# Performance work log

Measured on AMD Instinct MI355X. Metric: run time of the kernel, lower is better.

## Reference

```python
import jax, jax.numpy as jnp
import numpy as np

B_SZ, L, H, N, OUT = 16, 4096, 128, 64, 128  # batch, seq, channels(input_dim), state(hidden_dim), output_dim


def _hippo_legs(n):
    # HiPPO-LegS matrix: A[i,k] = -sqrt(2i+1)sqrt(2k+1) for i>k, -(i+1) on diag, 0 above.
    q = np.sqrt(2 * np.arange(n) + 1.0)
    A = -np.tril(np.outer(q, q), -1) - np.diag(np.arange(n) + 1.0)
    return A.astype(np.float32)


def setup_inputs() -> dict:
    key = jax.random.key(0)
    k1, k2, k3, k4, k5, k6, k7 = jax.random.split(key, 7)
    x = jax.random.normal(k1, (B_SZ, L, H), dtype=jnp.float32)
    A = jnp.asarray(_hippo_legs(N))                                   # (N, N) fixed HiPPO
    Bm = jax.random.normal(k2, (H, N), dtype=jnp.float32)             # per-channel input matrix
    Cm = jax.random.normal(k3, (H, N), dtype=jnp.float32)             # per-channel output matrix
    D = jax.random.normal(k4, (H,), dtype=jnp.float32)                # skip/feedthrough
    # log-uniform timescales in [1e-3, 1e-1]
    log_dt = jnp.log(jnp.float32(1e-3)) + jax.random.uniform(k5, (H,), dtype=jnp.float32) * (
        jnp.log(jnp.float32(1e-1)) - jnp.log(jnp.float32(1e-3)))
    W = jax.random.normal(k6, (OUT, H), dtype=jnp.float32) / np.sqrt(H)  # Linear(in=H, out=OUT) weight
    b = jax.random.normal(k7, (OUT,), dtype=jnp.float32) * 0.01
    return {"x": x, "A": A, "Bm": Bm, "Cm": Cm, "D": D, "log_dt": log_dt, "W": W, "b": b}


def reference(x, A, Bm, Cm, D, log_dt, W, b):
    n = A.shape[0]
    seq_len = x.shape[1]
    dt = jnp.exp(log_dt)[:, None, None]            # (H,1,1)
    I = jnp.eye(n, dtype=x.dtype)
    lhs = I[None] - 0.5 * dt * A[None]             # (H,N,N)
    rhs = I[None] + 0.5 * dt * A[None]
    A_bar = jnp.linalg.solve(lhs, rhs)             # bilinear discretization, per channel
    B_bar = jnp.linalg.solve(lhs, (dt[:, :, 0] * Bm)[..., None])[..., 0]  # (H,N)

    # SSM convolution kernel k_l = C A_bar^l B_bar via scan, vectorized over channels.
    def step(V, _):
        k = jnp.einsum('hn,hn->h', Cm, V)
        V = jnp.einsum('hmn,hn->hm', A_bar, V)
        return V, k

    _, ks = jax.lax.scan(step, B_bar, None, length=seq_len)  # (L, H)
    kernel = ks.T                                            # (H, L)

    # Causal convolution via FFT (the 'fourier' method).
    n_fft = 2 * seq_len
    Uf = jnp.fft.rfft(x, n=n_fft, axis=1)                    # (B, F, H)
    Kf = jnp.fft.rfft(kernel, n=n_fft, axis=1)               # (H, F)
    y = jnp.fft.irfft(Uf * Kf.T[None], n=n_fft, axis=1)[:, :seq_len, :]
    y = y + x * D[None, None, :]

    return y @ W.T + b
```

## Files before the change

### kernel.cpp

```cpp
#include <hip/hip_runtime.h>

#define BSZ   16
#define LSEQ  4096
#define HCH   128
#define NST   64
#define NOUTD 128
#define TCH   64
#define NCHK  64

typedef unsigned long long u64;

#define OFF_XT 0ull
#define OFF_U  8388608ull
#define OFF_S  16777216ull
#define OFF_G  25165824ull
#define OFF_M  25690112ull
#define OFF_P  26214400ull
#define OFF_K  26738688ull
#define OFF_WT 26746880ull

__global__ __launch_bounds__(256) void k_tr_x(const float* __restrict__ x, float* __restrict__ xT){
  __shared__ float tile[64][65];
  int l0 = blockIdx.x*64, h0 = blockIdx.y*64, b = blockIdx.z;
  int tid = threadIdx.x;
  int tl = tid>>6, th = tid&63;
  #pragma unroll
  for (int k=0;k<16;k++){
    int l = tl + k*4;
    tile[l][th] = x[((u64)b*LSEQ + l0+l)*HCH + h0+th];
  }
  __syncthreads();
  #pragma unroll
  for (int k=0;k<16;k++){
    int hh = tl + k*4;
    xT[((u64)b*HCH + h0+hh)*LSEQ + l0+th] = tile[th][hh];
  }
}

__global__ __launch_bounds__(256) void k_tr_w(const float* __restrict__ W, float* __restrict__ Wt){
  int idx = blockIdx.x*256 + threadIdx.x;
  int o = idx >> 7, h = idx & 127;
  Wt[h*NOUTD + o] = W[o*HCH + h];
}

__global__ __launch_bounds__(512) void k_pre(const float* __restrict__ A, const float* __restrict__ Bm,
                   const float* __restrict__ Cm, const float* __restrict__ log_dt,
                   float* __restrict__ G, float* __restrict__ Mx,
                   float* __restrict__ P, float* __restrict__ ks){
  __shared__ __align__(16) float Ls [64][68];
  __shared__ __align__(16) float LsT[64][68];
  __shared__ __align__(16) float Bb [64][68];
  __shared__ __align__(16) float BbT[64][68];
  __shared__ __align__(16) float Vt [64][68];
  __shared__ __align__(16) float Wt [64][68];
  __shared__ float vbuf[64];
  __shared__ float cbuf[64];
  const int h = blockIdx.x, tid = threadIdx.x;
  const int lane = tid & 63, wid = tid >> 6;
  const float dt = expf(log_dt[h]);

  for (int i = tid; i < 4096; i += 512){
    int r = i >> 6, c = i & 63;
    Ls[r][c] = ((r==c)?1.f:0.f) - 0.5f*dt*A[i];
  }
  if (tid < 64) vbuf[tid] = Bm[h*NST + tid];
  else if (tid < 128) cbuf[tid-64] = Cm[h*NST + (tid-64)];
  __syncthreads();

  float y[64];
  if (wid == 0){
    const int t = lane;
    #pragma unroll
    for (int j=0;j<64;j++) y[j] = 0.f;
    #pragma unroll
    for (int i=0;i<64;i++){
      float acc = ((i==t)?2.f:0.f) - Ls[i][t];
      #pragma unroll
      for (int j4=0;j4<(i+3)/4;j4++){
        float4 L4 = *(const float4*)&Ls[i][j4*4];
        acc -= L4.x*y[j4*4+0] + L4.y*y[j4*4+1] + L4.z*y[j4*4+2] + L4.w*y[j4*4+3];
      }
      y[i] = acc * (1.0f/Ls[i][i]);
    }
    #pragma unroll
    for (int i=0;i<64;i++){ Ls[i][t] = y[i]; LsT[t][i] = y[i]; }
  }
  __syncthreads();

  if (wid == 0){
    const int t = lane;
    float a0=0.f,a1=0.f,a2=0.f,a3=0.f;
    #pragma unroll
    for (int m4=0;m4<16;m4++){
      float4 r4 = *(const float4*)&Ls[t][m4*4];
      a0 += r4.x*vbuf[m4*4+0]; a1 += r4.y*vbuf[m4*4+1];
      a2 += r4.z*vbuf[m4*4+2]; a3 += r4.w*vbuf[m4*4+3];
    }
    Vt[0][t] = 0.5f*dt*(((a0+a1)+(a2+a3)) + vbuf[t]);
  } else if (wid == 1){
    const int n = lane;
    float a0=0.f,a1=0.f,a2=0.f,a3=0.f;
    #pragma unroll
    for (int m4=0;m4<16;m4++){
      float4 c4 = *(const float4*)&LsT[n][m4*4];
      a0 += c4.x*cbuf[m4*4+0]; a1 += c4.y*cbuf[m4*4+1];
      a2 += c4.z*cbuf[m4*4+2]; a3 += c4.w*cbuf[m4*4+3];
    }
    Wt[0][n] = (a0+a1)+(a2+a3);
  }
  __syncthreads();

  float (*cur)[68]  = Ls,  (*curT)[68] = LsT;
  float (*nxt)[68]  = Bb,  (*nxtT)[68] = BbT;
  for (int k=0;k<6;k++){
    const int nv = 1<<k;
    for (int j = tid; j < 32*nv; j += 512){
      const int isW = (j >= 16*nv);
      const int jj  = isW ? (j - 16*nv) : j;
      const int i   = jj >> 4;
      const int n0  = (jj & 15) << 2;
      float (*Xs)[68] = isW ? Wt  : Vt;
      float (*Ms)[68] = isW ? cur : curT;
      float o0=0.f,o1=0.f,o2=0.f,o3=0.f;
      #pragma unroll
      for (int m4=0;m4<16;m4++){
        const float4 xv = *(const float4*)&Xs[i][m4*4];
        const float4 c0 = *(const float4*)&Ms[m4*4+0][n0];
        const float4 c1 = *(const float4*)&Ms[m4*4+1][n0];
        const float4 c2 = *(const float4*)&Ms[m4*4+2][n0];
        const float4 c3 = *(const float4*)&Ms[m4*4+3][n0];
        o0 += xv.x*c0.x + xv.y*c1.x + xv.z*c2.x + xv.w*c3.x;
        o1 += xv.x*c0.y + xv.y*c1.y + xv.z*c2.y + xv.w*c3.y;
        o2 += xv.x*c0.z + xv.y*c1.z + xv.z*c2.z + xv.w*c3.z;
        o3 += xv.x*c0.w + xv.y*c1.w + xv.z*c2.w + xv.w*c3.w;
      }
      float* dst = isW ? &Wt[nv+i][n0] : &Vt[nv+i][n0];
      *(float4*)dst = make_float4(o0,o1,o2,o3);
    }
    {
      const int ti = (tid >> 4) << 1;
      const int tj = (tid & 15) << 2;
      float acc[2][4] = {};
      #pragma unroll
      for (int m4=0;m4<16;m4++){
        const float4 a0 = *(const float4*)&cur[ti+0][m4*4];
        const float4 a1 = *(const float4*)&cur[ti+1][m4*4];
        const float4 b0 = *(const float4*)&cur[m4*4+0][tj];
        const float4 b1 = *(const float4*)&cur[m4*4+1][tj];
        const float4 b2 = *(const float4*)&cur[m4*4+2][tj];
        const float4 b3 = *(const float4*)&cur[m4*4+3][tj];
        acc[0][0] += a0.x*b0.x + a0.y*b1.x + a0.z*b2.x + a0.w*b3.x;
        acc[0][1] += a0.x*b0.y + a0.y*b1.y + a0.z*b2.y + a0.w*b3.y;
        acc[0][2] += a0.x*b0.z + a0.y*b1.z + a0.z*b2.z + a0.w*b3.z;
        acc[0][3] += a0.x*b0.w + a0.y*b1.w + a0.z*b2.w + a0.w*b3.w;
        acc[1][0] += a1.x*b0.x + a1.y*b1.x + a1.z*b2.x + a1.w*b3.x;
        acc[1][1] += a1.x*b0.y + a1.y*b1.y + a1.z*b2.y + a1.w*b3.y;
        acc[1][2] += a1.x*b0.z + a1.y*b1.z + a1.z*b2.z + a1.w*b3.z;
        acc[1][3] += a1.x*b0.w + a1.y*b1.w + a1.z*b2.w + a1.w*b3.w;
      }
      *(float4*)&nxt[ti+0][tj] = make_float4(acc[0][0],acc[0][1],acc[0][2],acc[0][3]);
      *(float4*)&nxt[ti+1][tj] = make_float4(acc[1][0],acc[1][1],acc[1][2],acc[1][3]);
      #pragma unroll
      for (int e=0;e<4;e++){
        nxtT[tj+e][ti+0] = acc[0][e];
        nxtT[tj+e][ti+1] = acc[1][e];
      }
    }
    __syncthreads();
    { float (*t0)[68]=cur; cur=nxt;  nxt=t0; }
    { float (*t1)[68]=curT; curT=nxtT; nxtT=t1; }
  }

  if (wid == 0){
    const int j = lane;
    float a0=0.f,a1=0.f,a2=0.f,a3=0.f;
    #pragma unroll
    for (int n4=0;n4<16;n4++){
      float4 v4 = *(const float4*)&Vt[j][n4*4];
      a0 += v4.x*cbuf[n4*4+0]; a1 += v4.y*cbuf[n4*4+1];
      a2 += v4.z*cbuf[n4*4+2]; a3 += v4.w*cbuf[n4*4+3];
    }
    ks[h*64 + j] = (a0+a1)+(a2+a3);
  }
  for (int idx = tid; idx < 4096; idx += 512){
    const int t = idx >> 6, n = idx & 63;
    G [(u64)h*4096 + idx] = Vt[63-t][n];
    Mx[(u64)h*4096 + idx] = Wt[n][t];
    P [(u64)h*4096 + idx] = cur[t][n];
  }
}

__global__ __launch_bounds__(512) void k_ssm(const float* __restrict__ xT, const float* __restrict__ G,
                       const float* __restrict__ MxT, const float* __restrict__ P,
                       const float* __restrict__ ks, const float* __restrict__ D,
                       float* __restrict__ zT){
  __shared__ __align__(16) float xs[64][68];
  __shared__ __align__(16) float gs[64][68];
  __shared__ __align__(16) float us[64][68];
  __shared__ float kv[64];
  const int h = blockIdx.x, b = blockIdx.y;
  const int tid = threadIdx.x, lane = tid & 63, wid = tid >> 6;

  const float* xb = xT + ((u64)b*HCH + h)*LSEQ;
  const float* Mg = MxT + (u64)h*4096;
  if (tid < 64) kv[tid] = ks[h*64 + tid];
  for (int i = tid; i < 4096; i += 512){
    xs[i>>6][i&63] = xb[i];
    gs[i>>6][i&63] = G[(u64)h*4096 + i];
  }
  __syncthreads();

  const int tb = tid>>4, tn = tid&15;
  {
    float acc[2][4] = {};
    #pragma unroll 8
    for (int t=0;t<64;t++){
      float4 g4 = *(const float4*)&gs[t][tn*4];
      #pragma unroll
      for (int r=0;r<2;r++){
        float xv = xs[tb*2+r][t];
        acc[r][0] += xv*g4.x; acc[r][1] += xv*g4.y; acc[r][2] += xv*g4.z; acc[r][3] += xv*g4.w;
      }
    }
    #pragma unroll
    for (int r=0;r<2;r++)
      *(float4*)&us[tb*2+r][tn*4] = make_float4(acc[r][0],acc[r][1],acc[r][2],acc[r][3]);
  }
  __syncthreads();

  if (wid != 0){
    for (int i = tid-64; i < 4096; i += 448){
      int j = i>>6, t = i&63;
      gs[j][t] = (t>=j)? kv[t-j] : 0.f;
    }
  } else {
    const float* Ph = P + (u64)h*4096;
    float prow[64];
    #pragma unroll
    for (int j4=0;j4<16;j4++){
      float4 p4 = *(const float4*)&Ph[lane*64 + j4*4];
      prow[j4*4+0]=p4.x; prow[j4*4+1]=p4.y; prow[j4*4+2]=p4.z; prow[j4*4+3]=p4.w;
    }
    float s = 0.f;
    for (int c=0;c<NCHK;c++){
      float u = us[c][lane];
      us[c][lane] = s;
      float a0=u, a1=0.f, a2=0.f, a3=0.f;
      #pragma unroll
      for (int j4=0;j4<16;j4++){
        float s0 = __uint_as_float(__builtin_amdgcn_readlane(__float_as_uint(s), j4*4+0));
        float s1 = __uint_as_float(__builtin_amdgcn_readlane(__float_as_uint(s), j4*4+1));
        float s2 = __uint_as_float(__builtin_amdgcn_readlane(__float_as_uint(s), j4*4+2));
        float s3 = __uint_as_float(__builtin_amdgcn_readlane(__float_as_uint(s), j4*4+3));
        a0 += s0*prow[j4*4+0]; a1 += s1*prow[j4*4+1];
        a2 += s2*prow[j4*4+2]; a3 += s3*prow[j4*4+3];
      }
      s = (a0+a1)+(a2+a3);
    }
  }
  __syncthreads();

  {
    float acc[2][4] = {};
    #pragma unroll 4
    for (int kk=0;kk<64;kk++){
      float4 b4 = *(const float4*)&gs[kk][tn*4];
      #pragma unroll
      for (int r=0;r<2;r++){
        float av = xs[tb*2+r][kk];
        acc[r][0]+=av*b4.x; acc[r][1]+=av*b4.y; acc[r][2]+=av*b4.z; acc[r][3]+=av*b4.w;
      }
    }
    #pragma unroll 4
    for (int kk=0;kk<64;kk++){
      float4 b4 = *(const float4*)&Mg[kk*64 + tn*4];
      #pragma unroll
      for (int r=0;r<2;r++){
        float sv = us[tb*2+r][kk];
        acc[r][0]+=sv*b4.x; acc[r][1]+=sv*b4.y; acc[r][2]+=sv*b4.z; acc[r][3]+=sv*b4.w;
      }
    }
    const float dv = D[h];
    float* zb = zT + ((u64)b*HCH + h)*LSEQ;
    #pragma unroll
    for (int r=0;r<2;r++){
      int c = tb*2+r;
      float4 o4;
      o4.x = acc[r][0] + dv*xs[c][tn*4+0];
      o4.y = acc[r][1] + dv*xs[c][tn*4+1];
      o4.z = acc[r][2] + dv*xs[c][tn*4+2];
      o4.w = acc[r][3] + dv*xs[c][tn*4+3];
      *(float4*)&zb[c*64 + tn*4] = o4;
    }
  }
}

__global__ __launch_bounds__(256) void k_out(const float* __restrict__ zT, const float* __restrict__ Wt,
                       const float* __restrict__ bias, float* __restrict__ out){
  int l0 = blockIdx.x*64, b = blockIdx.y;
  __shared__ __align__(16) float zl[128][64];
  int tid = threadIdx.x;
  for (int i=tid;i<8192;i+=256){
    int hh=i>>6, ll=i&63;
    zl[hh][ll] = zT[((u64)b*HCH + hh)*LSEQ + l0 + ll];
  }
  __syncthreads();
  int lane = tid&63, wid = tid>>6;
  int o = (wid&1)*64 + lane;
  int lq0 = (wid>>1)*32;
  float bo = bias[o];
  float acc[32];
  #pragma unroll
  for (int q=0;q<32;q++) acc[q] = bo;
  #pragma unroll 2
  for (int hh=0;hh<128;hh++){
    float wv = Wt[hh*NOUTD + o];
    #pragma unroll
    for (int q4=0;q4<8;q4++){
      float4 z4 = *(const float4*)&zl[hh][lq0 + q4*4];
      acc[q4*4+0] += wv*z4.x; acc[q4*4+1] += wv*z4.y; acc[q4*4+2] += wv*z4.z; acc[q4*4+3] += wv*z4.w;
    }
  }
  #pragma unroll
  for (int q=0;q<32;q++){
    out[((u64)b*LSEQ + l0 + lq0 + q)*NOUTD + o] = acc[q];
  }
}

extern "C" void kernel_launch(void* const* d_in, const int* in_sizes, int n_in,
                              void* d_out, int out_size, void* d_ws, size_t ws_size,
                              hipStream_t stream){
  const float* x      = (const float*)d_in[0];
  const float* A      = (const float*)d_in[1];
  const float* Bm     = (const float*)d_in[2];
  const float* Cm     = (const float*)d_in[3];
  const float* D      = (const float*)d_in[4];
  const float* log_dt = (const float*)d_in[5];
  const float* W      = (const float*)d_in[6];
  const float* bias   = (const float*)d_in[7];
  float* out = (float*)d_out;
  float* ws  = (float*)d_ws;

  float* xT  = ws + OFF_XT;
  float* zT  = ws + OFF_U;
  float* G   = ws + OFF_G;
  float* MxT = ws + OFF_M;
  float* P   = ws + OFF_P;
  float* ks  = ws + OFF_K;
  float* Wt  = ws + OFF_WT;

  hipLaunchKernelGGL(k_tr_x, dim3(64,2,16), dim3(256), 0, stream, x, xT);
  hipLaunchKernelGGL(k_tr_w, dim3(64),      dim3(256), 0, stream, W, Wt);
  hipLaunchKernelGGL(k_pre,  dim3(128),     dim3(512), 0, stream, A, Bm, Cm, log_dt, G, MxT, P, ks);
  hipLaunchKernelGGL(k_ssm,  dim3(128,16),  dim3(512), 0, stream, xT, G, MxT, P, ks, D, zT);
  hipLaunchKernelGGL(k_out,  dim3(64,16),   dim3(256), 0, stream, zT, Wt, bias, out);
}
```

Before: 277.6 us.

## Drop x transpose kernel, prefetch Mx in registers, retile output GEMM

Removes the separate transpose pass over x. k_ssm now gathers its per-channel column straight from x with a stride of HCH, which drops a full read and write of the 32 MB input but makes that load uncoalesced. The Mx loop in k_ssm is software-pipelined with double-buffered float4 registers to hide global-load latency. k_out is retiled to a 4x8 register block per thread with float4 loads of W and float4 stores of the output, giving more reuse and wider stores.

```diff
diff --git a/kernel.cpp b/kernel.cpp
--- a/kernel.cpp
+++ b/kernel.cpp
@@ -12,30 +12,11 @@
 
 #define OFF_XT 0ull
 #define OFF_U  8388608ull
-#define OFF_S  16777216ull
 #define OFF_G  25165824ull
 #define OFF_M  25690112ull
 #define OFF_P  26214400ull
 #define OFF_K  26738688ull
 #define OFF_WT 26746880ull
-
-__global__ __launch_bounds__(256) void k_tr_x(const float* __restrict__ x, float* __restrict__ xT){
-  __shared__ float tile[64][65];
-  int l0 = blockIdx.x*64, h0 = blockIdx.y*64, b = blockIdx.z;
-  int tid = threadIdx.x;
-  int tl = tid>>6, th = tid&63;
-  #pragma unroll
-  for (int k=0;k<16;k++){
-    int l = tl + k*4;
-    tile[l][th] = x[((u64)b*LSEQ + l0+l)*HCH + h0+th];
-  }
-  __syncthreads();
-  #pragma unroll
-  for (int k=0;k<16;k++){
-    int hh = tl + k*4;
-    xT[((u64)b*HCH + h0+hh)*LSEQ + l0+th] = tile[th][hh];
-  }
-}
 
 __global__ __launch_bounds__(256) void k_tr_w(const float* __restrict__ W, float* __restrict__ Wt){
   int idx = blockIdx.x*256 + threadIdx.x;
@@ -190,7 +171,7 @@
   }
 }
 
-__global__ __launch_bounds__(512) void k_ssm(const float* __restrict__ xT, const float* __restrict__ G,
+__global__ __launch_bounds__(512) void k_ssm(const float* __restrict__ x, const float* __restrict__ G,
                        const float* __restrict__ MxT, const float* __restrict__ P,
                        const float* __restrict__ ks, const float* __restrict__ D,
                        float* __restrict__ zT){
@@ -201,11 +182,11 @@
   const int h = blockIdx.x, b = blockIdx.y;
   const int tid = threadIdx.x, lane = tid & 63, wid = tid >> 6;
 
-  const float* xb = xT + ((u64)b*HCH + h)*LSEQ;
+  const float* xg = x + (u64)b*LSEQ*HCH + h;
   const float* Mg = MxT + (u64)h*4096;
   if (tid < 64) kv[tid] = ks[h*64 + tid];
   for (int i = tid; i < 4096; i += 512){
-    xs[i>>6][i&63] = xb[i];
+    xs[i>>6][i&63] = xg[(u64)i*HCH];
     gs[i>>6][i&63] = G[(u64)h*4096 + i];
   }
   __syncthreads();
@@ -271,13 +252,40 @@
         acc[r][0]+=av*b4.x; acc[r][1]+=av*b4.y; acc[r][2]+=av*b4.z; acc[r][3]+=av*b4.w;
       }
     }
-    #pragma unroll 4
-    for (int kk=0;kk<64;kk++){
-      float4 b4 = *(const float4*)&Mg[kk*64 + tn*4];
-      #pragma unroll
-      for (int r=0;r<2;r++){
-        float sv = us[tb*2+r][kk];
-        acc[r][0]+=sv*b4.x; acc[r][1]+=sv*b4.y; acc[r][2]+=sv*b4.z; acc[r][3]+=sv*b4.w;
+    float4 ma[4], mb[4];
+    #pragma unroll
+    for (int p=0;p<4;p++) ma[p] = *(const float4*)&Mg[p*64 + tn*4];
+    #pragma unroll
+    for (int k0=0; k0<64; k0+=8){
+      #pragma unroll
+      for (int p=0;p<4;p++){
+        int kk = k0+4+p;
+        mb[p] = *(const float4*)&Mg[(kk<64? kk:0)*64 + tn*4];
+      }
+      #pragma unroll
+      for (int p=0;p<4;p++){
+        float4 b4 = ma[p];
+        int kk = k0+p;
+        #pragma unroll
+        for (int r=0;r<2;r++){
+          float sv = us[tb*2+r][kk];
+          acc[r][0]+=sv*b4.x; acc[r][1]+=sv*b4.y; acc[r][2]+=sv*b4.z; acc[r][3]+=sv*b4.w;
+        }
+      }
+      #pragma unroll
+      for (int p=0;p<4;p++){
+        int kk = k0+8+p;
+        ma[p] = *(const float4*)&Mg[(kk<64? kk:0)*64 + tn*4];
+      }
+      #pragma unroll
+      for (int p=0;p<4;p++){
+        float4 b4 = mb[p];
+        int kk = k0+4+p;
+        #pragma unroll
+        for (int r=0;r<2;r++){
+          float sv = us[tb*2+r][kk];
+          acc[r][0]+=sv*b4.x; acc[r][1]+=sv*b4.y; acc[r][2]+=sv*b4.z; acc[r][3]+=sv*b4.w;
+        }
       }
     }
     const float dv = D[h];
@@ -298,32 +306,41 @@
 __global__ __launch_bounds__(256) void k_out(const float* __restrict__ zT, const float* __restrict__ Wt,
                        const float* __restrict__ bias, float* __restrict__ out){
   int l0 = blockIdx.x*64, b = blockIdx.y;
-  __shared__ __align__(16) float zl[128][64];
+  __shared__ __align__(16) float4 zl4[128][16];
   int tid = threadIdx.x;
-  for (int i=tid;i<8192;i+=256){
-    int hh=i>>6, ll=i&63;
-    zl[hh][ll] = zT[((u64)b*HCH + hh)*LSEQ + l0 + ll];
-  }
-  __syncthreads();
-  int lane = tid&63, wid = tid>>6;
-  int o = (wid&1)*64 + lane;
-  int lq0 = (wid>>1)*32;
-  float bo = bias[o];
-  float acc[32];
+  for (int i = tid; i < 2048; i += 256){
+    int hh = i>>4, q = i&15;
+    zl4[hh][q] = *(const float4*)&zT[((u64)b*HCH + hh)*LSEQ + l0 + q*4];
+  }
+  __syncthreads();
+  const int lg = tid>>4;
+  const int og = tid&15;
+  float acc[4][8];
   #pragma unroll
-  for (int q=0;q<32;q++) acc[q] = bo;
-  #pragma unroll 2
-  for (int hh=0;hh<128;hh++){
-    float wv = Wt[hh*NOUTD + o];
-    #pragma unroll
-    for (int q4=0;q4<8;q4++){
-      float4 z4 = *(const float4*)&zl[hh][lq0 + q4*4];
-      acc[q4*4+0] += wv*z4.x; acc[q4*4+1] += wv*z4.y; acc[q4*4+2] += wv*z4.z; acc[q4*4+3] += wv*z4.w;
+  for (int e=0;e<8;e++){
+    float bo = bias[og*8+e];
+    #pragma unroll
+    for (int r=0;r<4;r++) acc[r][e] = bo;
+  }
+  #pragma unroll 4
+  for (int hh=0; hh<128; hh++){
+    float4 z4 = zl4[hh][lg];
+    float4 w0 = *(const float4*)&Wt[hh*NOUTD + og*8];
+    float4 w1 = *(const float4*)&Wt[hh*NOUTD + og*8 + 4];
+    float zr[4] = {z4.x, z4.y, z4.z, z4.w};
+    #pragma unroll
+    for (int r=0;r<4;r++){
+      acc[r][0] += zr[r]*w0.x; acc[r][1] += zr[r]*w0.y;
+      acc[r][2] += zr[r]*w0.z; acc[r][3] += zr[r]*w0.w;
+      acc[r][4] += zr[r]*w1.x; acc[r][5] += zr[r]*w1.y;
+      acc[r][6] += zr[r]*w1.z; acc[r][7] += zr[r]*w1.w;
     }
   }
   #pragma unroll
-  for (int q=0;q<32;q++){
-    out[((u64)b*LSEQ + l0 + lq0 + q)*NOUTD + o] = acc[q];
+  for (int r=0;r<4;r++){
+    u64 row = (u64)b*LSEQ + l0 + lg*4 + r;
+    *(float4*)&out[row*NOUTD + og*8]     = make_float4(acc[r][0],acc[r][1],acc[r][2],acc[r][3]);
+    *(float4*)&out[row*NOUTD + og*8 + 4] = make_float4(acc[r][4],acc[r][5],acc[r][6],acc[r][7]);
   }
 }
 
@@ -341,7 +358,6 @@
   float* out = (float*)d_out;
   float* ws  = (float*)d_ws;
 
-  float* xT  = ws + OFF_XT;
   float* zT  = ws + OFF_U;
   float* G   = ws + OFF_G;
   float* MxT = ws + OFF_M;
@@ -349,9 +365,8 @@
   float* ks  = ws + OFF_K;
   float* Wt  = ws + OFF_WT;
 
-  hipLaunchKernelGGL(k_tr_x, dim3(64,2,16), dim3(256), 0, stream, x, xT);
   hipLaunchKernelGGL(k_tr_w, dim3(64),      dim3(256), 0, stream, W, Wt);
   hipLaunchKernelGGL(k_pre,  dim3(128),     dim3(512), 0, stream, A, Bm, Cm, log_dt, G, MxT, P, ks);
-  hipLaunchKernelGGL(k_ssm,  dim3(128,16),  dim3(512), 0, stream, xT, G, MxT, P, ks, D, zT);
+  hipLaunchKernelGGL(k_ssm,  dim3(128,16),  dim3(512), 0, stream, x, G, MxT, P, ks, D, zT);
   hipLaunchKernelGGL(k_out,  dim3(64,16),   dim3(256), 0, stream, zT, Wt, bias, out);
 }
```

Result: slower. 288.7 us (+4.0%).
